# Optimization experiments

Hardware: AMD Instinct MI355X
Metric: run time of the kernel (lower is better)

The kernel has to match this reference:

```python
import jax, jax.numpy as jnp
import numpy as np

NUM_USERS = 100000
NUM_ITEMS = 50000
HIDDEN = 64
NUM_LAYERS = 3
NUM_EDGES = 1200000
N = NUM_USERS + NUM_ITEMS


def setup_inputs() -> dict:
    key = jax.random.key(0)
    k_e, k_u, k_i, k_w, k_b = jax.random.split(key, 5)
    edge_index = jax.random.randint(k_e, (2, NUM_EDGES), 0, N, dtype=jnp.int32)
    users_emb = jax.random.normal(k_u, (NUM_USERS, HIDDEN), dtype=jnp.float32) * 0.01
    items_emb = jax.random.normal(k_i, (NUM_ITEMS, HIDDEN), dtype=jnp.float32) * 0.01
    # GCNConv linear weights (glorot-ish) and zero biases, stacked over layers
    scale = 1.0 / np.sqrt(HIDDEN)
    Ws = jax.random.uniform(k_w, (NUM_LAYERS, HIDDEN, HIDDEN), dtype=jnp.float32,
                            minval=-scale, maxval=scale)
    bs = jnp.zeros((NUM_LAYERS, HIDDEN), dtype=jnp.float32)
    return {"edge_index": edge_index, "users_emb": users_emb,
            "items_emb": items_emb, "Ws": Ws, "bs": bs}


def reference(edge_index, users_emb, items_emb, Ws, bs):
    # GraphSAGEModel.forward: concat user/item embeddings, run num_layers GCNConv
    # (PyG defaults: add self-loops, symmetric D^-1/2 A D^-1/2 normalization, bias).
    x = jnp.concatenate([users_emb, items_emb], axis=0)  # [N, H]

    self_loops = jnp.arange(N, dtype=edge_index.dtype)
    src = jnp.concatenate([edge_index[0], self_loops])  # [E+N]
    dst = jnp.concatenate([edge_index[1], self_loops])

    ones = jnp.ones(src.shape[0], dtype=x.dtype)
    deg = jax.ops.segment_sum(ones, dst, num_segments=N)  # in-degree incl self loop
    dinv = jnp.where(deg > 0, jax.lax.rsqrt(deg), 0.0)
    norm = dinv[src] * dinv[dst]  # [E+N], graph-constant across layers

    for l in range(NUM_LAYERS):
        h = x @ Ws[l]                       # linear transform [N, H]
        msg = h[src] * norm[:, None]        # gather + scale
        x = jax.ops.segment_sum(msg, dst, num_segments=N) + bs[l]
    return (x[:NUM_USERS], users_emb, x[NUM_USERS:], items_emb)
```

## Files before the change

kernel.cpp:

```cpp
#include <hip/hip_runtime.h>
#include <hip/hip_fp16.h>

#define NU 100000
#define NI 50000
#define NN 150000
#define HH 64
#define NE 1200000

#define SCAN_CHUNK 1024
#define NBLK ((NN + SCAN_CHUNK - 1) / SCAN_CHUNK)
#define AGG_BLOCKS (NN / 8)

#define RANK_BLOCKS   ((NE / 8 + 255) / 256)
#define CONCAT4_BLOCKS (NN * 16 / 256)
#define FILL_BLOCKS   ((NE / 8 + 255) / 256)

__global__ __launch_bounds__(256) void k_rank_concat(
    const int4* __restrict__ dst4, int* __restrict__ counts, int4* __restrict__ rank4,
    const float4* __restrict__ users, const float4* __restrict__ items,
    __half2* __restrict__ xs, float4* __restrict__ out,
    __half* __restrict__ pad0, __half* __restrict__ pad1,
    float* __restrict__ dinv, float* __restrict__ p1u) {
    if (blockIdx.x < RANK_BLOCKS) {
        if (blockIdx.x == 0 && threadIdx.x < 18) {
            if (threadIdx.x < 8)       ((int4*)pad0)[threadIdx.x] = make_int4(0, 0, 0, 0);
            else if (threadIdx.x < 16) ((int4*)pad1)[threadIdx.x - 8] = make_int4(0, 0, 0, 0);
            else if (threadIdx.x == 16) dinv[NN] = 0.f;
            else                        p1u[NN] = 0.f;
        }
        int t = blockIdx.x * 256 + threadIdx.x;
        if (t >= NE / 8) return;
        int4 d0 = dst4[2 * t], d1 = dst4[2 * t + 1];
        int4 r0, r1;
        r0.x = atomicAdd(&counts[d0.x], 1);
        r0.y = atomicAdd(&counts[d0.y], 1);
        r0.z = atomicAdd(&counts[d0.z], 1);
        r0.w = atomicAdd(&counts[d0.w], 1);
        r1.x = atomicAdd(&counts[d1.x], 1);
        r1.y = atomicAdd(&counts[d1.y], 1);
        r1.z = atomicAdd(&counts[d1.z], 1);
        r1.w = atomicAdd(&counts[d1.w], 1);
        rank4[2 * t]     = r0;
        rank4[2 * t + 1] = r1;
    } else {
        int i = (blockIdx.x - RANK_BLOCKS) * 256 + threadIdx.x;
        const int UB = NU * 16;
        float4 v;
        if (i < UB) {
            v = users[i];
            out[UB + i] = v;
        } else {
            int j = i - UB;
            v = items[j];
            out[2 * UB + NI * 16 + j] = v;
        }
        xs[2 * i]     = __halves2half2(__float2half_rn(v.x), __float2half_rn(v.y));
        xs[2 * i + 1] = __halves2half2(__float2half_rn(v.z), __float2half_rn(v.w));
    }
}

__global__ __launch_bounds__(256) void k_scan(const int* __restrict__ counts,
                                              float* __restrict__ dinv,
                                              float* __restrict__ dinv2,
                                              int* __restrict__ row_ptr,
                                              unsigned int* __restrict__ state,
                                              const float* __restrict__ Wfull,
                                              const float* __restrict__ bfull,
                                              float* __restrict__ What,
                                              float* __restrict__ cvec) {
    __shared__ float smem[HH * HH];
    __shared__ int s_prefix;
    int t = threadIdx.x;
    int b = blockIdx.x;

    if (b == NBLK) {
        int r = t >> 2, j0 = (t & 3) * 16;
        const float* W0 = Wfull;
        const float* W1 = Wfull + HH * HH;
        const float* W2 = Wfull + 2 * HH * HH;
        float acc[16];
#pragma unroll
        for (int j = 0; j < 16; ++j) acc[j] = 0.f;
        for (int k = 0; k < HH; ++k) {
            float a = W1[r * HH + k];
            const float* bp = W2 + k * HH + j0;
#pragma unroll
            for (int j = 0; j < 16; ++j) acc[j] += a * bp[j];
        }
#pragma unroll
        for (int j = 0; j < 16; ++j) smem[r * HH + j0 + j] = acc[j];
        if (t < HH) {
            float s = 0.f;
            for (int k = 0; k < HH; ++k) s += bfull[HH + k] * W2[k * HH + t];
            cvec[HH + t] = s;
        }
        __syncthreads();
#pragma unroll
        for (int j = 0; j < 16; ++j) acc[j] = 0.f;
        for (int k = 0; k < HH; ++k) {
            float a = W0[r * HH + k];
            const float* bp = smem + k * HH + j0;
#pragma unroll
            for (int j = 0; j < 16; ++j) acc[j] += a * bp[j];
        }
#pragma unroll
        for (int j = 0; j < 16; ++j) What[r * HH + j0 + j] = acc[j];
        if (t < HH) {
            float s = 0.f;
            for (int k = 0; k < HH; ++k) s += bfull[k] * smem[k * HH + t];
            cvec[t] = s;
        }
        return;
    }

    int* sd = (int*)smem;
    int base = b * SCAN_CHUNK + t * 4;
    int c[4];
    if (base + 3 < NN) {
        int4 v = *(const int4*)(counts + base);
        c[0] = v.x; c[1] = v.y; c[2] = v.z; c[3] = v.w;
    } else {
#pragma unroll
        for (int i = 0; i < 4; ++i) c[i] = (base + i < NN) ? counts[base + i] : 0;
    }
#pragma unroll
    for (int i = 0; i < 4; ++i)
        if (base + i < NN) {
            dinv[base + i]  = rsqrtf((float)(c[i] + 1));
            dinv2[base + i] = 1.0f / (float)(c[i] + 1);
        }

    int tt = c[0] + c[1] + c[2] + c[3];
    sd[t] = tt; __syncthreads();
    for (int off = 1; off < 256; off <<= 1) {
        int x = (t >= off) ? sd[t - off] : 0;
        __syncthreads();
        sd[t] += x;
        __syncthreads();
    }

    if (t == 0) {
        unsigned int agg = (unsigned int)sd[255];
        if (b == 0) {
            __hip_atomic_store(&state[0], (2u << 30) | agg, __ATOMIC_RELEASE,
                               __HIP_MEMORY_SCOPE_AGENT);
            s_prefix = 0;
        } else {
            __hip_atomic_store(&state[b], (1u << 30) | agg, __ATOMIC_RELEASE,
                               __HIP_MEMORY_SCOPE_AGENT);
            unsigned int prefix = 0;
            int p = b - 1;
            while (true) {
                unsigned int s = __hip_atomic_load(&state[p], __ATOMIC_ACQUIRE,
                                                   __HIP_MEMORY_SCOPE_AGENT);
                unsigned int fl = s >> 30;
                if (fl == 0u) { __builtin_amdgcn_s_sleep(1); continue; }
                prefix += s & 0x3FFFFFFFu;
                if (fl == 2u) break;
                --p;
            }
            __hip_atomic_store(&state[b], (2u << 30) | (prefix + agg),
                               __ATOMIC_RELEASE, __HIP_MEMORY_SCOPE_AGENT);
            s_prefix = (int)prefix;
        }
    }
    __syncthreads();

    int off0 = s_prefix + (sd[t] - tt);
    int run = 0;
#pragma unroll
    for (int i = 0; i < 4; ++i) {
        if (base + i < NN) row_ptr[base + i] = off0 + run;
        run += c[i];
    }
    if (b == NBLK - 1 && t == 0) row_ptr[NN] = NE;
}

__global__ __launch_bounds__(256) void k_fill(const int4* __restrict__ src4,
                                              const int4* __restrict__ dst4,
                                              const int4* __restrict__ rank4,
                                              const int* __restrict__ row_ptr,
                                              int* __restrict__ col) {
    int t = blockIdx.x * 256 + threadIdx.x;
    if (t >= NE / 8) return;
    int4 s0 = src4[2 * t],  s1 = src4[2 * t + 1];
    int4 d0 = dst4[2 * t],  d1 = dst4[2 * t + 1];
    int4 r0 = rank4[2 * t], r1 = rank4[2 * t + 1];
    int p0 = row_ptr[d0.x], p1 = row_ptr[d0.y], p2 = row_ptr[d0.z], p3 = row_ptr[d0.w];
    int p4 = row_ptr[d1.x], p5 = row_ptr[d1.y], p6 = row_ptr[d1.z], p7 = row_ptr[d1.w];
    col[p0 + r0.x] = s0.x;
    col[p1 + r0.y] = s0.y;
    col[p2 + r0.z] = s0.z;
    col[p3 + r0.w] = s0.w;
    col[p4 + r1.x] = s1.x;
    col[p5 + r1.y] = s1.y;
    col[p6 + r1.z] = s1.z;
    col[p7 + r1.w] = s1.w;
}

template <int UMODE>
__global__ __launch_bounds__(256) void k_aggregate(
    const __half* __restrict__ x, __half* __restrict__ y,
    const float* __restrict__ scale,
    const int* __restrict__ row_ptr, const int* __restrict__ col,
    const float* __restrict__ dinv, const float* __restrict__ pin,
    float* __restrict__ uout, float* __restrict__ pout) {
    int lane = threadIdx.x & 63;
    int wave = blockIdx.x * 4 + (threadIdx.x >> 6);
    int na = wave * 2;
    if (na >= NN) return;
    int nb = na + 1;
    int o  = lane >> 3;
    int f8 = (lane & 7) << 3;

    float a[8], b[8];
#pragma unroll
    for (int j = 0; j < 8; ++j) { a[j] = 0.f; b[j] = 0.f; }
    float ua = 0.f, ub = 0.f;

#define GATHER(r, acc, uacc)                                               \
    {                                                                      \
        int4 raw = *(const int4*)(x + (size_t)(r) * HH + f8);              \
        float dr = 1.f;                                                    \
        if (UMODE) { dr = pin[r]; uacc += dr; }                            \
        __half2* hp = (__half2*)&raw;                                      \
        _Pragma("unroll")                                                  \
        for (int j = 0; j < 4; ++j) {                                      \
            float2 f = __half22float2(hp[j]);                              \
            if (UMODE == 1) { acc[2 * j] += dr * f.x; acc[2 * j + 1] += dr * f.y; } \
            else            { acc[2 * j] += f.x;      acc[2 * j + 1] += f.y; }      \
        }                                                                  \
    }

    int ea = row_ptr[na], enda = row_ptr[na + 1];
    int eb = enda,        endb = row_ptr[nb + 1];

    {
        int ia = ea + o - 1;
        int ib = eb + o - 1;
        int rA = (o == 0) ? na : ((ia < enda) ? col[ia] : NN);
        int rB = (o == 0) ? nb : ((ib < endb) ? col[ib] : NN);
        GATHER(rA, a, ua);
        GATHER(rB, b, ub);
        ea += 7; eb += 7;
    }
    while (ea < enda || eb < endb) {
        int iA0 = ea + o,     iA1 = ea + 8 + o;
        int iB0 = eb + o,     iB1 = eb + 8 + o;
        int rA0 = (iA0 < enda) ? col[iA0] : NN;
        int rA1 = (iA1 < enda) ? col[iA1] : NN;
        int rB0 = (iB0 < endb) ? col[iB0] : NN;
        int rB1 = (iB1 < endb) ? col[iB1] : NN;
        GATHER(rA0, a, ua);
        GATHER(rA1, a, ua);
        GATHER(rB0, b, ub);
        GATHER(rB1, b, ub);
        ea += 16; eb += 16;
    }
#undef GATHER

#pragma unroll
    for (int j = 0; j < 8; ++j) {
        a[j] += __shfl_xor(a[j], 8);  b[j] += __shfl_xor(b[j], 8);
        a[j] += __shfl_xor(a[j], 16); b[j] += __shfl_xor(b[j], 16);
        a[j] += __shfl_xor(a[j], 32); b[j] += __shfl_xor(b[j], 32);
    }
    if (UMODE) {
        ua += __shfl_xor(ua, 8);  ub += __shfl_xor(ub, 8);
        ua += __shfl_xor(ua, 16); ub += __shfl_xor(ub, 16);
        ua += __shfl_xor(ua, 32); ub += __shfl_xor(ub, 32);
    }

    if (o < 2) {
        int   n  = (o == 0) ? na : nb;
        float dv = scale[n];
        __half2 h[4];
#pragma unroll
        for (int j = 0; j < 4; ++j) {
            float x0 = (o == 0) ? a[2 * j]     : b[2 * j];
            float x1 = (o == 0) ? a[2 * j + 1] : b[2 * j + 1];
            h[j] = __halves2half2(__float2half_rn(dv * x0), __float2half_rn(dv * x1));
        }
        *(int4*)(y + (size_t)n * HH + f8) = *(int4*)h;
    }
    if (UMODE && lane < 2) {
        int n = na + lane;
        float s = ((lane == 0) ? ua : ub) * 0.125f;
        float dvn = dinv[n];
        float u = dvn * s;
        uout[n] = u;
        if (UMODE == 1) pout[n] = dvn * u;
    }
}

#define GR 128
#define XSS 65
__global__ __launch_bounds__(256) void k_gemm_final(
    const __half* __restrict__ y, const float* __restrict__ W,
    const float* __restrict__ b2, const float* __restrict__ cvec,
    const float* __restrict__ u1, const float* __restrict__ u2,
    float* __restrict__ out_lo, float* __restrict__ out_hi) {
    __shared__ float xs[GR * XSS];
    __shared__ float ws[HH * HH];
    int t = threadIdx.x;
    int rowBase = blockIdx.x * GR;

    {
        const float4* W4 = (const float4*)W;
        float4* ws4 = (float4*)ws;
#pragma unroll
        for (int i = 0; i < 4; ++i) ws4[i * 256 + t] = W4[i * 256 + t];
    }
#pragma unroll
    for (int it = 0; it < 4; ++it) {
        int g = it * 256 + t;
        int r = g >> 3;
        int c0 = (g & 7) * 8;
        int row = rowBase + r;
        if (row < NN) {
            int4 raw = *(const int4*)(y + (size_t)row * HH + c0);
            __half2 h0 = *(__half2*)&raw.x, h1 = *(__half2*)&raw.y;
            __half2 h2 = *(__half2*)&raw.z, h3 = *(__half2*)&raw.w;
            float2 f0 = __half22float2(h0), f1 = __half22float2(h1);
            float2 f2 = __half22float2(h2), f3 = __half22float2(h3);
            float* dp = xs + r * XSS + c0;
            dp[0] = f0.x; dp[1] = f0.y; dp[2] = f1.x; dp[3] = f1.y;
            dp[4] = f2.x; dp[5] = f2.y; dp[6] = f3.x; dp[7] = f3.y;
        }
    }
    __syncthreads();

    int tx = t & 7;
    int ty = t >> 3;
    int j0 = tx * 8;
    int r0 = ty * 4;

    float acc[4][8];
#pragma unroll
    for (int i = 0; i < 4; ++i)
#pragma unroll
        for (int j = 0; j < 8; ++j) acc[i][j] = 0.f;

    for (int k = 0; k < HH; ++k) {
        float4 w0 = *(const float4*)(ws + k * HH + j0);
        float4 w1 = *(const float4*)(ws + k * HH + j0 + 4);
        float wv[8] = {w0.x, w0.y, w0.z, w0.w, w1.x, w1.y, w1.z, w1.w};
#pragma unroll
        for (int i = 0; i < 4; ++i) {
            float xv = xs[(r0 + i) * XSS + k];
#pragma unroll
            for (int j = 0; j < 8; ++j) acc[i][j] += xv * wv[j];
        }
    }

    float c0j[8], c1j[8], b2j[8];
#pragma unroll
    for (int j = 0; j < 8; ++j) {
        c0j[j] = cvec[j0 + j];
        c1j[j] = cvec[HH + j0 + j];
        b2j[j] = b2[j0 + j];
    }

#pragma unroll
    for (int i = 0; i < 4; ++i) {
        int r = rowBase + r0 + i;
        if (r >= NN) continue;
        float u2r = u2[r], u1r = u1[r];
        float base[8];
#pragma unroll
        for (int j = 0; j < 8; ++j) base[j] = u2r * c0j[j] + u1r * c1j[j] + b2j[j];
        float4 o0 = make_float4(acc[i][0] + base[0], acc[i][1] + base[1],
                                acc[i][2] + base[2], acc[i][3] + base[3]);
        float4 o1 = make_float4(acc[i][4] + base[4], acc[i][5] + base[5],
                                acc[i][6] + base[6], acc[i][7] + base[7]);
        float* d = (r < NU) ? (out_lo + (size_t)r * HH)
                            : (out_hi + (size_t)(r - NU) * HH);
        *(float4*)(d + j0) = o0;
        *(float4*)(d + j0 + 4) = o1;
    }
}

extern "C" void kernel_launch(void* const* d_in, const int* in_sizes, int n_in,
                              void* d_out, int out_size, void* d_ws, size_t ws_size,
                              hipStream_t stream) {
    const int*   edge  = (const int*)d_in[0];
    const int*   src   = edge;
    const int*   dst   = edge + NE;
    const float* users = (const float*)d_in[1];
    const float* items = (const float*)d_in[2];
    const float* Ws    = (const float*)d_in[3];
    const float* bs    = (const float*)d_in[4];
    float*       out   = (float*)d_out;

    char* w = (char*)d_ws;
    __half* Xs0     = (__half*)w; w += (size_t)(NN + 1) * HH * 2;
    __half* Xs1     = (__half*)w; w += (size_t)(NN + 1) * HH * 2;
    float*  dinv    = (float*)w;  w += (size_t)(NN + 1) * 4;
    float*  dinv2   = (float*)w;  w += (size_t)NN * 4;
    float*  u1      = (float*)w;  w += (size_t)NN * 4;
    float*  p1u     = (float*)w;  w += (size_t)(NN + 1) * 4;
    float*  u2      = (float*)w;  w += (size_t)NN * 4;
    float*  What    = (float*)w;  w += (size_t)HH * HH * 4;
    float*  cvec    = (float*)w;  w += (size_t)2 * HH * 4;
    unsigned int* state = (unsigned int*)w; w += 256 * 4;
    int*    counts  = (int*)w;    w += (size_t)NN * 4;
    int*    row_ptr = (int*)w;    w += (size_t)(NN + 1) * 4;
    w += 12;
    int*    col     = (int*)w;    w += (size_t)NE * 4;
    int*    rank    = (int*)w;    w += (size_t)NE * 4;
    (void)ws_size; (void)in_sizes; (void)n_in; (void)out_size;

    hipMemsetAsync(state, 0, (size_t)(256 + NN) * sizeof(int), stream);

    k_rank_concat<<<RANK_BLOCKS + CONCAT4_BLOCKS, 256, 0, stream>>>(
        (const int4*)dst, counts, (int4*)rank,
        (const float4*)users, (const float4*)items, (__half2*)Xs0, (float4*)out,
        Xs0 + (size_t)NN * HH, Xs1 + (size_t)NN * HH, dinv, p1u);
    k_scan<<<NBLK + 1, 256, 0, stream>>>(counts, dinv, dinv2, row_ptr, state,
                                         Ws, bs, What, cvec);
    k_fill<<<FILL_BLOCKS, 256, 0, stream>>>(
        (const int4*)src, (const int4*)dst, (const int4*)rank, row_ptr, col);

    k_aggregate<1><<<AGG_BLOCKS, 256, 0, stream>>>(
        Xs0, Xs1, dinv2, row_ptr, col, dinv, dinv, u1, p1u);
    k_aggregate<2><<<AGG_BLOCKS, 256, 0, stream>>>(
        Xs1, Xs0, dinv2, row_ptr, col, dinv, p1u, u2, nullptr);
    k_aggregate<0><<<AGG_BLOCKS, 256, 0, stream>>>(
        Xs0, Xs1, dinv, row_ptr, col, nullptr, nullptr, nullptr, nullptr);

    const int GEMM_BLOCKS = (NN + GR - 1) / GR;
    k_gemm_final<<<GEMM_BLOCKS, 256, 0, stream>>>(
        Xs1, What, bs + 2 * HH, cvec, u1, u2,
        out , out + (size_t)2 * NU * HH );
}
```

Measured before the change: 403.0 us.

## Fuse CSR fill into scan via grid barrier; fuse last aggregation into final GEMM

```diff
diff --git a/kernel.cpp b/kernel.cpp
--- a/kernel.cpp
+++ b/kernel.cpp
@@ -9,11 +9,11 @@
 
 #define SCAN_CHUNK 1024
 #define NBLK ((NN + SCAN_CHUNK - 1) / SCAN_CHUNK)
+#define SCAN_GRID (NBLK + 1)
 #define AGG_BLOCKS (NN / 8)
 
 #define RANK_BLOCKS   ((NE / 8 + 255) / 256)
 #define CONCAT4_BLOCKS (NN * 16 / 256)
-#define FILL_BLOCKS   ((NE / 8 + 255) / 256)
 
 __global__ __launch_bounds__(256) void k_rank_concat(
     const int4* __restrict__ dst4, int* __restrict__ counts, int4* __restrict__ rank4,
@@ -59,15 +59,14 @@
     }
 }
 
-__global__ __launch_bounds__(256) void k_scan(const int* __restrict__ counts,
-                                              float* __restrict__ dinv,
-                                              float* __restrict__ dinv2,
-                                              int* __restrict__ row_ptr,
-                                              unsigned int* __restrict__ state,
-                                              const float* __restrict__ Wfull,
-                                              const float* __restrict__ bfull,
-                                              float* __restrict__ What,
-                                              float* __restrict__ cvec) {
+__global__ __launch_bounds__(256) void k_scan_fill(
+    const int* __restrict__ counts,
+    float* __restrict__ dinv, float* __restrict__ dinv2,
+    int* __restrict__ row_ptr, unsigned int* __restrict__ state,
+    const float* __restrict__ Wfull, const float* __restrict__ bfull,
+    float* __restrict__ What, float* __restrict__ cvec,
+    const int4* __restrict__ src4, const int4* __restrict__ dst4,
+    const int4* __restrict__ rank4, int* __restrict__ col) {
     __shared__ float smem[HH * HH];
     __shared__ int s_prefix;
     int t = threadIdx.x;
@@ -110,92 +109,97 @@
             for (int k = 0; k < HH; ++k) s += bfull[k] * smem[k * HH + t];
             cvec[t] = s;
         }
-        return;
-    }
-
-    int* sd = (int*)smem;
-    int base = b * SCAN_CHUNK + t * 4;
-    int c[4];
-    if (base + 3 < NN) {
-        int4 v = *(const int4*)(counts + base);
-        c[0] = v.x; c[1] = v.y; c[2] = v.z; c[3] = v.w;
     } else {
-#pragma unroll
-        for (int i = 0; i < 4; ++i) c[i] = (base + i < NN) ? counts[base + i] : 0;
-    }
-#pragma unroll
-    for (int i = 0; i < 4; ++i)
-        if (base + i < NN) {
-            dinv[base + i]  = rsqrtf((float)(c[i] + 1));
-            dinv2[base + i] = 1.0f / (float)(c[i] + 1);
-        }
-
-    int tt = c[0] + c[1] + c[2] + c[3];
-    sd[t] = tt; __syncthreads();
-    for (int off = 1; off < 256; off <<= 1) {
-        int x = (t >= off) ? sd[t - off] : 0;
+        int* sd = (int*)smem;
+        int base = b * SCAN_CHUNK + t * 4;
+        int c[4];
+        if (base + 3 < NN) {
+            int4 v = *(const int4*)(counts + base);
+            c[0] = v.x; c[1] = v.y; c[2] = v.z; c[3] = v.w;
+        } else {
+#pragma unroll
+            for (int i = 0; i < 4; ++i) c[i] = (base + i < NN) ? counts[base + i] : 0;
+        }
+#pragma unroll
+        for (int i = 0; i < 4; ++i)
+            if (base + i < NN) {
+                dinv[base + i]  = rsqrtf((float)(c[i] + 1));
+                dinv2[base + i] = 1.0f / (float)(c[i] + 1);
+            }
+
+        int tt = c[0] + c[1] + c[2] + c[3];
+        sd[t] = tt; __syncthreads();
+        for (int off = 1; off < 256; off <<= 1) {
+            int x = (t >= off) ? sd[t - off] : 0;
+            __syncthreads();
+            sd[t] += x;
+            __syncthreads();
+        }
+
+        if (t == 0) {
+            unsigned int agg = (unsigned int)sd[255];
+            if (b == 0) {
+                __hip_atomic_store(&state[0], (2u << 30) | agg, __ATOMIC_RELEASE,
+                                   __HIP_MEMORY_SCOPE_AGENT);
+                s_prefix = 0;
+            } else {
+                __hip_atomic_store(&state[b], (1u << 30) | agg, __ATOMIC_RELEASE,
+                                   __HIP_MEMORY_SCOPE_AGENT);
+                unsigned int prefix = 0;
+                int p = b - 1;
+                while (true) {
+                    unsigned int s = __hip_atomic_load(&state[p], __ATOMIC_ACQUIRE,
+                                                       __HIP_MEMORY_SCOPE_AGENT);
+                    unsigned int fl = s >> 30;
+                    if (fl == 0u) { __builtin_amdgcn_s_sleep(1); continue; }
+                    prefix += s & 0x3FFFFFFFu;
+                    if (fl == 2u) break;
+                    --p;
+                }
+                __hip_atomic_store(&state[b], (2u << 30) | (prefix + agg),
+                                   __ATOMIC_RELEASE, __HIP_MEMORY_SCOPE_AGENT);
+                s_prefix = (int)prefix;
+            }
+        }
         __syncthreads();
-        sd[t] += x;
-        __syncthreads();
-    }
-
+
+        int off0 = s_prefix + (sd[t] - tt);
+        int run = 0;
+#pragma unroll
+        for (int i = 0; i < 4; ++i) {
+            if (base + i < NN) row_ptr[base + i] = off0 + run;
+            run += c[i];
+        }
+        if (b == NBLK - 1 && t == 0) row_ptr[NN] = NE;
+    }
+
+    unsigned int* done = state + 192;
+    __threadfence();
+    __syncthreads();
     if (t == 0) {
-        unsigned int agg = (unsigned int)sd[255];
-        if (b == 0) {
-            __hip_atomic_store(&state[0], (2u << 30) | agg, __ATOMIC_RELEASE,
-                               __HIP_MEMORY_SCOPE_AGENT);
-            s_prefix = 0;
-        } else {
-            __hip_atomic_store(&state[b], (1u << 30) | agg, __ATOMIC_RELEASE,
-                               __HIP_MEMORY_SCOPE_AGENT);
-            unsigned int prefix = 0;
-            int p = b - 1;
-            while (true) {
-                unsigned int s = __hip_atomic_load(&state[p], __ATOMIC_ACQUIRE,
-                                                   __HIP_MEMORY_SCOPE_AGENT);
-                unsigned int fl = s >> 30;
-                if (fl == 0u) { __builtin_amdgcn_s_sleep(1); continue; }
-                prefix += s & 0x3FFFFFFFu;
-                if (fl == 2u) break;
-                --p;
-            }
-            __hip_atomic_store(&state[b], (2u << 30) | (prefix + agg),
-                               __ATOMIC_RELEASE, __HIP_MEMORY_SCOPE_AGENT);
-            s_prefix = (int)prefix;
-        }
+        __hip_atomic_fetch_add(done, 1u, __ATOMIC_ACQ_REL, __HIP_MEMORY_SCOPE_AGENT);
+        while (__hip_atomic_load(done, __ATOMIC_ACQUIRE, __HIP_MEMORY_SCOPE_AGENT)
+               < (unsigned int)SCAN_GRID)
+            __builtin_amdgcn_s_sleep(4);
     }
     __syncthreads();
-
-    int off0 = s_prefix + (sd[t] - tt);
-    int run = 0;
-#pragma unroll
-    for (int i = 0; i < 4; ++i) {
-        if (base + i < NN) row_ptr[base + i] = off0 + run;
-        run += c[i];
-    }
-    if (b == NBLK - 1 && t == 0) row_ptr[NN] = NE;
-}
-
-__global__ __launch_bounds__(256) void k_fill(const int4* __restrict__ src4,
-                                              const int4* __restrict__ dst4,
-                                              const int4* __restrict__ rank4,
-                                              const int* __restrict__ row_ptr,
-                                              int* __restrict__ col) {
-    int t = blockIdx.x * 256 + threadIdx.x;
-    if (t >= NE / 8) return;
-    int4 s0 = src4[2 * t],  s1 = src4[2 * t + 1];
-    int4 d0 = dst4[2 * t],  d1 = dst4[2 * t + 1];
-    int4 r0 = rank4[2 * t], r1 = rank4[2 * t + 1];
-    int p0 = row_ptr[d0.x], p1 = row_ptr[d0.y], p2 = row_ptr[d0.z], p3 = row_ptr[d0.w];
-    int p4 = row_ptr[d1.x], p5 = row_ptr[d1.y], p6 = row_ptr[d1.z], p7 = row_ptr[d1.w];
-    col[p0 + r0.x] = s0.x;
-    col[p1 + r0.y] = s0.y;
-    col[p2 + r0.z] = s0.z;
-    col[p3 + r0.w] = s0.w;
-    col[p4 + r1.x] = s1.x;
-    col[p5 + r1.y] = s1.y;
-    col[p6 + r1.z] = s1.z;
-    col[p7 + r1.w] = s1.w;
+    __threadfence();
+
+    for (int e = b * 256 + t; e < NE / 8; e += SCAN_GRID * 256) {
+        int4 s0 = src4[2 * e],  s1 = src4[2 * e + 1];
+        int4 d0 = dst4[2 * e],  d1 = dst4[2 * e + 1];
+        int4 r0 = rank4[2 * e], r1 = rank4[2 * e + 1];
+        int p0 = row_ptr[d0.x], p1 = row_ptr[d0.y], p2 = row_ptr[d0.z], p3 = row_ptr[d0.w];
+        int p4 = row_ptr[d1.x], p5 = row_ptr[d1.y], p6 = row_ptr[d1.z], p7 = row_ptr[d1.w];
+        col[p0 + r0.x] = s0.x;
+        col[p1 + r0.y] = s0.y;
+        col[p2 + r0.z] = s0.z;
+        col[p3 + r0.w] = s0.w;
+        col[p4 + r1.x] = s1.x;
+        col[p5 + r1.y] = s1.y;
+        col[p6 + r1.z] = s1.z;
+        col[p7 + r1.w] = s1.w;
+    }
 }
 
 template <int UMODE>
@@ -294,10 +298,12 @@
 }
 
 #define GR 128
-#define XSS 65
-__global__ __launch_bounds__(256) void k_gemm_final(
-    const __half* __restrict__ y, const float* __restrict__ W,
-    const float* __restrict__ b2, const float* __restrict__ cvec,
+#define XSS 68
+__global__ __launch_bounds__(256) void k_agg_gemm(
+    const __half* __restrict__ x, const float* __restrict__ dinv,
+    const int* __restrict__ row_ptr, const int* __restrict__ col,
+    const float* __restrict__ W, const float* __restrict__ b2,
+    const float* __restrict__ cvec,
     const float* __restrict__ u1, const float* __restrict__ u2,
     float* __restrict__ out_lo, float* __restrict__ out_hi) {
     __shared__ float xs[GR * XSS];
@@ -311,21 +317,77 @@
 #pragma unroll
         for (int i = 0; i < 4; ++i) ws4[i * 256 + t] = W4[i * 256 + t];
     }
-#pragma unroll
-    for (int it = 0; it < 4; ++it) {
-        int g = it * 256 + t;
-        int r = g >> 3;
-        int c0 = (g & 7) * 8;
-        int row = rowBase + r;
-        if (row < NN) {
-            int4 raw = *(const int4*)(y + (size_t)row * HH + c0);
-            __half2 h0 = *(__half2*)&raw.x, h1 = *(__half2*)&raw.y;
-            __half2 h2 = *(__half2*)&raw.z, h3 = *(__half2*)&raw.w;
-            float2 f0 = __half22float2(h0), f1 = __half22float2(h1);
-            float2 f2 = __half22float2(h2), f3 = __half22float2(h3);
-            float* dp = xs + r * XSS + c0;
-            dp[0] = f0.x; dp[1] = f0.y; dp[2] = f1.x; dp[3] = f1.y;
-            dp[4] = f2.x; dp[5] = f2.y; dp[6] = f3.x; dp[7] = f3.y;
+
+    int lane = t & 63;
+    int wv   = t >> 6;
+    int o    = lane >> 3;
+    int f8   = (lane & 7) << 3;
+    for (int s = 0; s < GR / 8; ++s) {
+        int na = rowBase + s * 8 + wv * 2;
+        if (na >= NN) break;
+        int nb = na + 1;
+        float a[8], b[8];
+#pragma unroll
+        for (int j = 0; j < 8; ++j) { a[j] = 0.f; b[j] = 0.f; }
+
+#define GATHER(r, acc)                                                     \
+        {                                                                  \
+            int4 raw = *(const int4*)(x + (size_t)(r) * HH + f8);          \
+            __half2* hp = (__half2*)&raw;                                  \
+            _Pragma("unroll")                                              \
+            for (int j = 0; j < 4; ++j) {                                  \
+                float2 f = __half22float2(hp[j]);                          \
+                acc[2 * j] += f.x; acc[2 * j + 1] += f.y;                  \
+            }                                                              \
+        }
+
+        int ea = row_ptr[na], enda = row_ptr[na + 1];
+        int eb = enda,        endb = row_ptr[nb + 1];
+        {
+            int ia = ea + o - 1;
+            int ib = eb + o - 1;
+            int rA = (o == 0) ? na : ((ia < enda) ? col[ia] : NN);
+            int rB = (o == 0) ? nb : ((ib < endb) ? col[ib] : NN);
+            GATHER(rA, a);
+            GATHER(rB, b);
+            ea += 7; eb += 7;
+        }
+        while (ea < enda || eb < endb) {
+            int iA0 = ea + o,     iA1 = ea + 8 + o;
+            int iB0 = eb + o,     iB1 = eb + 8 + o;
+            int rA0 = (iA0 < enda) ? col[iA0] : NN;
+            int rA1 = (iA1 < enda) ? col[iA1] : NN;
+            int rB0 = (iB0 < endb) ? col[iB0] : NN;
+            int rB1 = (iB1 < endb) ? col[iB1] : NN;
+            GATHER(rA0, a);
+            GATHER(rA1, a);
+            GATHER(rB0, b);
+            GATHER(rB1, b);
+            ea += 16; eb += 16;
+        }
+#undef GATHER
+
+#pragma unroll
+        for (int j = 0; j < 8; ++j) {
+            a[j] += __shfl_xor(a[j], 8);  b[j] += __shfl_xor(b[j], 8);
+            a[j] += __shfl_xor(a[j], 16); b[j] += __shfl_xor(b[j], 16);
+            a[j] += __shfl_xor(a[j], 32); b[j] += __shfl_xor(b[j], 32);
+        }
+        if (o < 2) {
+            int n = (o == 0) ? na : nb;
+            float dv = dinv[n];
+            float* dp = xs + (n - rowBase) * XSS + f8;
+            float4 o0, o1;
+            o0.x = dv * ((o == 0) ? a[0] : b[0]);
+            o0.y = dv * ((o == 0) ? a[1] : b[1]);
+            o0.z = dv * ((o == 0) ? a[2] : b[2]);
+            o0.w = dv * ((o == 0) ? a[3] : b[3]);
+            o1.x = dv * ((o == 0) ? a[4] : b[4]);
+            o1.y = dv * ((o == 0) ? a[5] : b[5]);
+            o1.z = dv * ((o == 0) ? a[6] : b[6]);
+            o1.w = dv * ((o == 0) ? a[7] : b[7]);
+            *(float4*)dp = o0;
+            *(float4*)(dp + 4) = o1;
         }
     }
     __syncthreads();
@@ -344,12 +406,12 @@
     for (int k = 0; k < HH; ++k) {
         float4 w0 = *(const float4*)(ws + k * HH + j0);
         float4 w1 = *(const float4*)(ws + k * HH + j0 + 4);
-        float wv[8] = {w0.x, w0.y, w0.z, w0.w, w1.x, w1.y, w1.z, w1.w};
+        float wvv[8] = {w0.x, w0.y, w0.z, w0.w, w1.x, w1.y, w1.z, w1.w};
 #pragma unroll
         for (int i = 0; i < 4; ++i) {
             float xv = xs[(r0 + i) * XSS + k];
 #pragma unroll
-            for (int j = 0; j < 8; ++j) acc[i][j] += xv * wv[j];
+            for (int j = 0; j < 8; ++j) acc[i][j] += xv * wvv[j];
         }
     }
 
@@ -416,20 +478,17 @@
         (const int4*)dst, counts, (int4*)rank,
         (const float4*)users, (const float4*)items, (__half2*)Xs0, (float4*)out,
         Xs0 + (size_t)NN * HH, Xs1 + (size_t)NN * HH, dinv, p1u);
-    k_scan<<<NBLK + 1, 256, 0, stream>>>(counts, dinv, dinv2, row_ptr, state,
-                                         Ws, bs, What, cvec);
-    k_fill<<<FILL_BLOCKS, 256, 0, stream>>>(
-        (const int4*)src, (const int4*)dst, (const int4*)rank, row_ptr, col);
+    k_scan_fill<<<SCAN_GRID, 256, 0, stream>>>(
+        counts, dinv, dinv2, row_ptr, state, Ws, bs, What, cvec,
+        (const int4*)src, (const int4*)dst, (const int4*)rank, col);
 
     k_aggregate<1><<<AGG_BLOCKS, 256, 0, stream>>>(
         Xs0, Xs1, dinv2, row_ptr, col, dinv, dinv, u1, p1u);
     k_aggregate<2><<<AGG_BLOCKS, 256, 0, stream>>>(
         Xs1, Xs0, dinv2, row_ptr, col, dinv, p1u, u2, nullptr);
-    k_aggregate<0><<<AGG_BLOCKS, 256, 0, stream>>>(
-        Xs0, Xs1, dinv, row_ptr, col, nullptr, nullptr, nullptr, nullptr);
 
     const int GEMM_BLOCKS = (NN + GR - 1) / GR;
-    k_gemm_final<<<GEMM_BLOCKS, 256, 0, stream>>>(
-        Xs1, What, bs + 2 * HH, cvec, u1, u2,
+    k_agg_gemm<<<GEMM_BLOCKS, 256, 0, stream>>>(
+        Xs0, dinv, row_ptr, col, What, bs + 2 * HH, cvec, u1, u2,
         out , out + (size_t)2 * NU * HH );
 }
```

Measured after the change: 476.9 us. 18.3% more time.

## Fuse scan and CSR fill via grid barrier, interleave rank blocks, persistent aggregation

Applied to the files above, without the earlier changes.

```diff
diff --git a/kernel.cpp b/kernel.cpp
--- a/kernel.cpp
+++ b/kernel.cpp
@@ -9,11 +9,12 @@
 
 #define SCAN_CHUNK 1024
 #define NBLK ((NN + SCAN_CHUNK - 1) / SCAN_CHUNK)
-#define AGG_BLOCKS (NN / 8)
-
-#define RANK_BLOCKS   ((NE / 8 + 255) / 256)
-#define CONCAT4_BLOCKS (NN * 16 / 256)
-#define FILL_BLOCKS   ((NE / 8 + 255) / 256)
+#define SCAN_GRID (NBLK + 1)
+
+#define RANK_BLOCKS  ((NE / 8 + 255) / 256)
+#define RC_GRID 10000
+#define AGG_GRID 2048
+#define NPAIRS (NN / 2)
 
 __global__ __launch_bounds__(256) void k_rank_concat(
     const int4* __restrict__ dst4, int* __restrict__ counts, int4* __restrict__ rank4,
@@ -21,14 +22,17 @@
     __half2* __restrict__ xs, float4* __restrict__ out,
     __half* __restrict__ pad0, __half* __restrict__ pad1,
     float* __restrict__ dinv, float* __restrict__ p1u) {
-    if (blockIdx.x < RANK_BLOCKS) {
-        if (blockIdx.x == 0 && threadIdx.x < 18) {
+    int bid = blockIdx.x;
+    if ((bid & 15) == 0) {
+        int rb = bid >> 4;
+        if (rb >= RANK_BLOCKS) return;
+        if (rb == 0 && threadIdx.x < 18) {
             if (threadIdx.x < 8)       ((int4*)pad0)[threadIdx.x] = make_int4(0, 0, 0, 0);
             else if (threadIdx.x < 16) ((int4*)pad1)[threadIdx.x - 8] = make_int4(0, 0, 0, 0);
             else if (threadIdx.x == 16) dinv[NN] = 0.f;
             else                        p1u[NN] = 0.f;
         }
-        int t = blockIdx.x * 256 + threadIdx.x;
+        int t = rb * 256 + threadIdx.x;
         if (t >= NE / 8) return;
         int4 d0 = dst4[2 * t], d1 = dst4[2 * t + 1];
         int4 r0, r1;
@@ -43,7 +47,8 @@
         rank4[2 * t]     = r0;
         rank4[2 * t + 1] = r1;
     } else {
-        int i = (blockIdx.x - RANK_BLOCKS) * 256 + threadIdx.x;
+        int cb = bid - (bid >> 4) - 1;
+        int i = cb * 256 + threadIdx.x;
         const int UB = NU * 16;
         float4 v;
         if (i < UB) {
@@ -59,15 +64,14 @@
     }
 }
 
-__global__ __launch_bounds__(256) void k_scan(const int* __restrict__ counts,
-                                              float* __restrict__ dinv,
-                                              float* __restrict__ dinv2,
-                                              int* __restrict__ row_ptr,
-                                              unsigned int* __restrict__ state,
-                                              const float* __restrict__ Wfull,
-                                              const float* __restrict__ bfull,
-                                              float* __restrict__ What,
-                                              float* __restrict__ cvec) {
+__global__ __launch_bounds__(256) void k_scan_fill(
+    const int* __restrict__ counts,
+    float* __restrict__ dinv, float* __restrict__ dinv2,
+    int* __restrict__ row_ptr, unsigned int* __restrict__ state,
+    const float* __restrict__ Wfull, const float* __restrict__ bfull,
+    float* __restrict__ What, float* __restrict__ cvec,
+    const int4* __restrict__ src4, const int4* __restrict__ dst4,
+    const int4* __restrict__ rank4, int* __restrict__ col) {
     __shared__ float smem[HH * HH];
     __shared__ int s_prefix;
     int t = threadIdx.x;
@@ -110,92 +114,97 @@
             for (int k = 0; k < HH; ++k) s += bfull[k] * smem[k * HH + t];
             cvec[t] = s;
         }
-        return;
-    }
-
-    int* sd = (int*)smem;
-    int base = b * SCAN_CHUNK + t * 4;
-    int c[4];
-    if (base + 3 < NN) {
-        int4 v = *(const int4*)(counts + base);
-        c[0] = v.x; c[1] = v.y; c[2] = v.z; c[3] = v.w;
     } else {
-#pragma unroll
-        for (int i = 0; i < 4; ++i) c[i] = (base + i < NN) ? counts[base + i] : 0;
-    }
-#pragma unroll
-    for (int i = 0; i < 4; ++i)
-        if (base + i < NN) {
-            dinv[base + i]  = rsqrtf((float)(c[i] + 1));
-            dinv2[base + i] = 1.0f / (float)(c[i] + 1);
-        }
-
-    int tt = c[0] + c[1] + c[2] + c[3];
-    sd[t] = tt; __syncthreads();
-    for (int off = 1; off < 256; off <<= 1) {
-        int x = (t >= off) ? sd[t - off] : 0;
+        int* sd = (int*)smem;
+        int base = b * SCAN_CHUNK + t * 4;
+        int c[4];
+        if (base + 3 < NN) {
+            int4 v = *(const int4*)(counts + base);
+            c[0] = v.x; c[1] = v.y; c[2] = v.z; c[3] = v.w;
+        } else {
+#pragma unroll
+            for (int i = 0; i < 4; ++i) c[i] = (base + i < NN) ? counts[base + i] : 0;
+        }
+#pragma unroll
+        for (int i = 0; i < 4; ++i)
+            if (base + i < NN) {
+                dinv[base + i]  = rsqrtf((float)(c[i] + 1));
+                dinv2[base + i] = 1.0f / (float)(c[i] + 1);
+            }
+
+        int tt = c[0] + c[1] + c[2] + c[3];
+        sd[t] = tt; __syncthreads();
+        for (int off = 1; off < 256; off <<= 1) {
+            int x = (t >= off) ? sd[t - off] : 0;
+            __syncthreads();
+            sd[t] += x;
+            __syncthreads();
+        }
+
+        if (t == 0) {
+            unsigned int agg = (unsigned int)sd[255];
+            if (b == 0) {
+                __hip_atomic_store(&state[0], (2u << 30) | agg, __ATOMIC_RELEASE,
+                                   __HIP_MEMORY_SCOPE_AGENT);
+                s_prefix = 0;
+            } else {
+                __hip_atomic_store(&state[b], (1u << 30) | agg, __ATOMIC_RELEASE,
+                                   __HIP_MEMORY_SCOPE_AGENT);
+                unsigned int prefix = 0;
+                int p = b - 1;
+                while (true) {
+                    unsigned int s = __hip_atomic_load(&state[p], __ATOMIC_ACQUIRE,
+                                                       __HIP_MEMORY_SCOPE_AGENT);
+                    unsigned int fl = s >> 30;
+                    if (fl == 0u) { __builtin_amdgcn_s_sleep(1); continue; }
+                    prefix += s & 0x3FFFFFFFu;
+                    if (fl == 2u) break;
+                    --p;
+                }
+                __hip_atomic_store(&state[b], (2u << 30) | (prefix + agg),
+                                   __ATOMIC_RELEASE, __HIP_MEMORY_SCOPE_AGENT);
+                s_prefix = (int)prefix;
+            }
+        }
         __syncthreads();
-        sd[t] += x;
-        __syncthreads();
-    }
-
+
+        int off0 = s_prefix + (sd[t] - tt);
+        int run = 0;
+#pragma unroll
+        for (int i = 0; i < 4; ++i) {
+            if (base + i < NN) row_ptr[base + i] = off0 + run;
+            run += c[i];
+        }
+        if (b == NBLK - 1 && t == 0) row_ptr[NN] = NE;
+    }
+
+    unsigned int* done = state + 192;
+    __threadfence();
+    __syncthreads();
     if (t == 0) {
-        unsigned int agg = (unsigned int)sd[255];
-        if (b == 0) {
-            __hip_atomic_store(&state[0], (2u << 30) | agg, __ATOMIC_RELEASE,
-                               __HIP_MEMORY_SCOPE_AGENT);
-            s_prefix = 0;
-        } else {
-            __hip_atomic_store(&state[b], (1u << 30) | agg, __ATOMIC_RELEASE,
-                               __HIP_MEMORY_SCOPE_AGENT);
-            unsigned int prefix = 0;
-            int p = b - 1;
-            while (true) {
-                unsigned int s = __hip_atomic_load(&state[p], __ATOMIC_ACQUIRE,
-                                                   __HIP_MEMORY_SCOPE_AGENT);
-                unsigned int fl = s >> 30;
-                if (fl == 0u) { __builtin_amdgcn_s_sleep(1); continue; }
-                prefix += s & 0x3FFFFFFFu;
-                if (fl == 2u) break;
-                --p;
-            }
-            __hip_atomic_store(&state[b], (2u << 30) | (prefix + agg),
-                               __ATOMIC_RELEASE, __HIP_MEMORY_SCOPE_AGENT);
-            s_prefix = (int)prefix;
-        }
+        __hip_atomic_fetch_add(done, 1u, __ATOMIC_ACQ_REL, __HIP_MEMORY_SCOPE_AGENT);
+        while (__hip_atomic_load(done, __ATOMIC_ACQUIRE, __HIP_MEMORY_SCOPE_AGENT)
+               < (unsigned int)SCAN_GRID)
+            __builtin_amdgcn_s_sleep(4);
     }
     __syncthreads();
-
-    int off0 = s_prefix + (sd[t] - tt);
-    int run = 0;
-#pragma unroll
-    for (int i = 0; i < 4; ++i) {
-        if (base + i < NN) row_ptr[base + i] = off0 + run;
-        run += c[i];
-    }
-    if (b == NBLK - 1 && t == 0) row_ptr[NN] = NE;
-}
-
-__global__ __launch_bounds__(256) void k_fill(const int4* __restrict__ src4,
-                                              const int4* __restrict__ dst4,
-                                              const int4* __restrict__ rank4,
-                                              const int* __restrict__ row_ptr,
-                                              int* __restrict__ col) {
-    int t = blockIdx.x * 256 + threadIdx.x;
-    if (t >= NE / 8) return;
-    int4 s0 = src4[2 * t],  s1 = src4[2 * t + 1];
-    int4 d0 = dst4[2 * t],  d1 = dst4[2 * t + 1];
-    int4 r0 = rank4[2 * t], r1 = rank4[2 * t + 1];
-    int p0 = row_ptr[d0.x], p1 = row_ptr[d0.y], p2 = row_ptr[d0.z], p3 = row_ptr[d0.w];
-    int p4 = row_ptr[d1.x], p5 = row_ptr[d1.y], p6 = row_ptr[d1.z], p7 = row_ptr[d1.w];
-    col[p0 + r0.x] = s0.x;
-    col[p1 + r0.y] = s0.y;
-    col[p2 + r0.z] = s0.z;
-    col[p3 + r0.w] = s0.w;
-    col[p4 + r1.x] = s1.x;
-    col[p5 + r1.y] = s1.y;
-    col[p6 + r1.z] = s1.z;
-    col[p7 + r1.w] = s1.w;
+    __threadfence();
+
+    for (int e = b * 256 + t; e < NE / 8; e += SCAN_GRID * 256) {
+        int4 s0 = src4[2 * e],  s1 = src4[2 * e + 1];
+        int4 d0 = dst4[2 * e],  d1 = dst4[2 * e + 1];
+        int4 r0 = rank4[2 * e], r1 = rank4[2 * e + 1];
+        int p0 = row_ptr[d0.x], p1 = row_ptr[d0.y], p2 = row_ptr[d0.z], p3 = row_ptr[d0.w];
+        int p4 = row_ptr[d1.x], p5 = row_ptr[d1.y], p6 = row_ptr[d1.z], p7 = row_ptr[d1.w];
+        col[p0 + r0.x] = s0.x;
+        col[p1 + r0.y] = s0.y;
+        col[p2 + r0.z] = s0.z;
+        col[p3 + r0.w] = s0.w;
+        col[p4 + r1.x] = s1.x;
+        col[p5 + r1.y] = s1.y;
+        col[p6 + r1.z] = s1.z;
+        col[p7 + r1.w] = s1.w;
+    }
 }
 
 template <int UMODE>
@@ -206,90 +215,93 @@
     const float* __restrict__ dinv, const float* __restrict__ pin,
     float* __restrict__ uout, float* __restrict__ pout) {
     int lane = threadIdx.x & 63;
-    int wave = blockIdx.x * 4 + (threadIdx.x >> 6);
-    int na = wave * 2;
-    if (na >= NN) return;
-    int nb = na + 1;
+    int waveId = blockIdx.x * 4 + (threadIdx.x >> 6);
+    const int NW = AGG_GRID * 4;
     int o  = lane >> 3;
     int f8 = (lane & 7) << 3;
 
-    float a[8], b[8];
-#pragma unroll
-    for (int j = 0; j < 8; ++j) { a[j] = 0.f; b[j] = 0.f; }
-    float ua = 0.f, ub = 0.f;
+    for (int pair = waveId; pair < NPAIRS; pair += NW) {
+        int na = pair * 2;
+        int nb = na + 1;
+
+        float a[8], b[8];
+#pragma unroll
+        for (int j = 0; j < 8; ++j) { a[j] = 0.f; b[j] = 0.f; }
+        float ua = 0.f, ub = 0.f;
 
 #define GATHER(r, acc, uacc)                                               \
-    {                                                                      \
-        int4 raw = *(const int4*)(x + (size_t)(r) * HH + f8);              \
-        float dr = 1.f;                                                    \
-        if (UMODE) { dr = pin[r]; uacc += dr; }                            \
-        __half2* hp = (__half2*)&raw;                                      \
-        _Pragma("unroll")                                                  \
-        for (int j = 0; j < 4; ++j) {                                      \
-            float2 f = __half22float2(hp[j]);                              \
-            if (UMODE == 1) { acc[2 * j] += dr * f.x; acc[2 * j + 1] += dr * f.y; } \
-            else            { acc[2 * j] += f.x;      acc[2 * j + 1] += f.y; }      \
-        }                                                                  \
-    }
-
-    int ea = row_ptr[na], enda = row_ptr[na + 1];
-    int eb = enda,        endb = row_ptr[nb + 1];
-
-    {
-        int ia = ea + o - 1;
-        int ib = eb + o - 1;
-        int rA = (o == 0) ? na : ((ia < enda) ? col[ia] : NN);
-        int rB = (o == 0) ? nb : ((ib < endb) ? col[ib] : NN);
-        GATHER(rA, a, ua);
-        GATHER(rB, b, ub);
-        ea += 7; eb += 7;
-    }
-    while (ea < enda || eb < endb) {
-        int iA0 = ea + o,     iA1 = ea + 8 + o;
-        int iB0 = eb + o,     iB1 = eb + 8 + o;
-        int rA0 = (iA0 < enda) ? col[iA0] : NN;
-        int rA1 = (iA1 < enda) ? col[iA1] : NN;
-        int rB0 = (iB0 < endb) ? col[iB0] : NN;
-        int rB1 = (iB1 < endb) ? col[iB1] : NN;
-        GATHER(rA0, a, ua);
-        GATHER(rA1, a, ua);
-        GATHER(rB0, b, ub);
-        GATHER(rB1, b, ub);
-        ea += 16; eb += 16;
-    }
+        {                                                                  \
+            int4 raw = *(const int4*)(x + (size_t)(r) * HH + f8);          \
+            float dr = 1.f;                                                \
+            if (UMODE) { dr = pin[r]; uacc += dr; }                        \
+            __half2* hp = (__half2*)&raw;                                  \
+            _Pragma("unroll")                                              \
+            for (int j = 0; j < 4; ++j) {                                  \
+                float2 f = __half22float2(hp[j]);                          \
+                if (UMODE == 1) { acc[2 * j] += dr * f.x; acc[2 * j + 1] += dr * f.y; } \
+                else            { acc[2 * j] += f.x;      acc[2 * j + 1] += f.y; }      \
+            }                                                              \
+        }
+
+        int ea = row_ptr[na], enda = row_ptr[na + 1];
+        int eb = enda,        endb = row_ptr[nb + 1];
+
+        {
+            int ia = ea + o - 1;
+            int ib = eb + o - 1;
+            int rA = (o == 0) ? na : ((ia < enda) ? col[ia] : NN);
+            int rB = (o == 0) ? nb : ((ib < endb) ? col[ib] : NN);
+            GATHER(rA, a, ua);
+            GATHER(rB, b, ub);
+            ea += 7; eb += 7;
+        }
+        while (ea < enda || eb < endb) {
+            int iA0 = ea + o,     iA1 = ea + 8 + o;
+            int iB0 = eb + o,     iB1 = eb + 8 + o;
+            int rA0 = (iA0 < enda) ? col[iA0] : NN;
+            int rA1 = (iA1 < enda) ? col[iA1] : NN;
+            int rB0 = (iB0 < endb) ? col[iB0] : NN;
+            int rB1 = (iB1 < endb) ? col[iB1] : NN;
+            GATHER(rA0, a, ua);
+            GATHER(rA1, a, ua);
+            GATHER(rB0, b, ub);
+            GATHER(rB1, b, ub);
+            ea += 16; eb += 16;
+        }
 #undef GATHER
 
 #pragma unroll
-    for (int j = 0; j < 8; ++j) {
-        a[j] += __shfl_xor(a[j], 8);  b[j] += __shfl_xor(b[j], 8);
-        a[j] += __shfl_xor(a[j], 16); b[j] += __shfl_xor(b[j], 16);
-        a[j] += __shfl_xor(a[j], 32); b[j] += __shfl_xor(b[j], 32);
-    }
-    if (UMODE) {
-        ua += __shfl_xor(ua, 8);  ub += __shfl_xor(ub, 8);
-        ua += __shfl_xor(ua, 16); ub += __shfl_xor(ub, 16);
-        ua += __shfl_xor(ua, 32); ub += __shfl_xor(ub, 32);
-    }
-
-    if (o < 2) {
-        int   n  = (o == 0) ? na : nb;
-        float dv = scale[n];
-        __half2 h[4];
-#pragma unroll
-        for (int j = 0; j < 4; ++j) {
-            float x0 = (o == 0) ? a[2 * j]     : b[2 * j];
-            float x1 = (o == 0) ? a[2 * j + 1] : b[2 * j + 1];
-            h[j] = __halves2half2(__float2half_rn(dv * x0), __float2half_rn(dv * x1));
-        }
-        *(int4*)(y + (size_t)n * HH + f8) = *(int4*)h;
-    }
-    if (UMODE && lane < 2) {
-        int n = na + lane;
-        float s = ((lane == 0) ? ua : ub) * 0.125f;
-        float dvn = dinv[n];
-        float u = dvn * s;
-        uout[n] = u;
-        if (UMODE == 1) pout[n] = dvn * u;
+        for (int j = 0; j < 8; ++j) {
+            a[j] += __shfl_xor(a[j], 8);  b[j] += __shfl_xor(b[j], 8);
+            a[j] += __shfl_xor(a[j], 16); b[j] += __shfl_xor(b[j], 16);
+            a[j] += __shfl_xor(a[j], 32); b[j] += __shfl_xor(b[j], 32);
+        }
+        if (UMODE) {
+            ua += __shfl_xor(ua, 8);  ub += __shfl_xor(ub, 8);
+            ua += __shfl_xor(ua, 16); ub += __shfl_xor(ub, 16);
+            ua += __shfl_xor(ua, 32); ub += __shfl_xor(ub, 32);
+        }
+
+        if (o < 2) {
+            int   n  = (o == 0) ? na : nb;
+            float dv = scale[n];
+            __half2 h[4];
+#pragma unroll
+            for (int j = 0; j < 4; ++j) {
+                float x0 = (o == 0) ? a[2 * j]     : b[2 * j];
+                float x1 = (o == 0) ? a[2 * j + 1] : b[2 * j + 1];
+                h[j] = __halves2half2(__float2half_rn(dv * x0), __float2half_rn(dv * x1));
+            }
+            *(int4*)(y + (size_t)n * HH + f8) = *(int4*)h;
+        }
+        if (UMODE && lane < 2) {
+            int n = na + lane;
+            float s = ((lane == 0) ? ua : ub) * 0.125f;
+            float dvn = dinv[n];
+            float u = dvn * s;
+            uout[n] = u;
+            if (UMODE == 1) pout[n] = dvn * u;
+        }
     }
 }
 
@@ -412,20 +424,19 @@
 
     hipMemsetAsync(state, 0, (size_t)(256 + NN) * sizeof(int), stream);
 
-    k_rank_concat<<<RANK_BLOCKS + CONCAT4_BLOCKS, 256, 0, stream>>>(
+    k_rank_concat<<<RC_GRID, 256, 0, stream>>>(
         (const int4*)dst, counts, (int4*)rank,
         (const float4*)users, (const float4*)items, (__half2*)Xs0, (float4*)out,
         Xs0 + (size_t)NN * HH, Xs1 + (size_t)NN * HH, dinv, p1u);
-    k_scan<<<NBLK + 1, 256, 0, stream>>>(counts, dinv, dinv2, row_ptr, state,
-                                         Ws, bs, What, cvec);
-    k_fill<<<FILL_BLOCKS, 256, 0, stream>>>(
-        (const int4*)src, (const int4*)dst, (const int4*)rank, row_ptr, col);
-
-    k_aggregate<1><<<AGG_BLOCKS, 256, 0, stream>>>(
+    k_scan_fill<<<SCAN_GRID, 256, 0, stream>>>(
+        counts, dinv, dinv2, row_ptr, state, Ws, bs, What, cvec,
+        (const int4*)src, (const int4*)dst, (const int4*)rank, col);
+
+    k_aggregate<1><<<AGG_GRID, 256, 0, stream>>>(
         Xs0, Xs1, dinv2, row_ptr, col, dinv, dinv, u1, p1u);
-    k_aggregate<2><<<AGG_BLOCKS, 256, 0, stream>>>(
+    k_aggregate<2><<<AGG_GRID, 256, 0, stream>>>(
         Xs1, Xs0, dinv2, row_ptr, col, dinv, p1u, u2, nullptr);
-    k_aggregate<0><<<AGG_BLOCKS, 256, 0, stream>>>(
+    k_aggregate<0><<<AGG_GRID, 256, 0, stream>>>(
         Xs0, Xs1, dinv, row_ptr, col, nullptr, nullptr, nullptr, nullptr);
 
     const int GEMM_BLOCKS = (NN + GR - 1) / GR;
```

Measured after the change: 573.7 us. +42.4%, slower.
